# Optimization experiments

Measured on AMD Instinct MI355X. Metric: run time of the kernel, lower is better.

## Reference

```python
import jax, jax.numpy as jnp
import numpy as np


def _outer(a, b):
    # 2D cross product z-component: a.x*b.y - a.y*b.x, elementwise over [..., 2]
    return a[..., 0] * b[..., 1] - a[..., 1] * b[..., 0]


def setup_inputs() -> dict:
    key = jax.random.key(0)
    P, L = 8192, 3072  # paths, points per path; L = 3*C with C curves
    points = jax.random.normal(key, (P, L, 2), dtype=jnp.float32)
    return {"points": points}


def reference(points) -> jnp.ndarray:
    # points: [P, L, 2], L = 3*C. Curve i uses points[3i], [3i+1], [3i+2],
    # and p4 = points[3i+3] (wrapping to points[0] for the last curve).
    p1 = points[:, 0::3]                 # [P, C, 2]
    p2 = points[:, 1::3]                 # [P, C, 2]
    p3 = points[:, 2::3]                 # [P, C, 2]
    p4 = jnp.roll(p1, -1, axis=1)        # [P, C, 2]; wraps last curve to points[0]

    v12 = p2 - p1
    v23 = p3 - p2
    v43 = p4 - p3

    # D1: hard sign test (1 if outer > 0 else 0), matching the torch branch
    D1 = (_outer(v12, v23) > 0).astype(points.dtype)  # [P, C]
    # D2: normalized outer product between first and last control segments
    D2 = _outer(v12, v43) / (
        jnp.linalg.norm(v12, axis=-1) * jnp.linalg.norm(v43, axis=-1)
    )                                                   # [P, C]

    xings = D1 * jax.nn.relu(-D2) + (1.0 - D1) * jax.nn.relu(D2)
    return jnp.mean(xings)
```

## Files before the change

### kernel.cpp

```cpp
#include <hip/hip_runtime.h>


#define NTHREADS 256
#define NBLOCKS  2048
#define ROW_FLOATS 6144
#define ITEMS_PER_ROW 256

__device__ __forceinline__ float xing1(float p1x, float p1y, float p2x, float p2y,
                                       float p3x, float p3y, float p4x, float p4y) {
    float v12x = p2x - p1x, v12y = p2y - p1y;
    float v23x = p3x - p2x, v23y = p3y - p2y;
    float v43x = p4x - p3x, v43y = p4y - p3y;
    float c1 = v12x * v23y - v12y * v23x;
    float c2 = v12x * v43y - v12y * v43x;
    float d12 = v12x * v12x + v12y * v12y;
    float d43 = v43x * v43x + v43y * v43y;
    float inv = __builtin_amdgcn_rsqf(d12 * d43);
    float s = (c1 > 0.0f) ? -c2 : c2;
    return fmaxf(s * inv, 0.0f);
}

__global__ __launch_bounds__(NTHREADS) void xing_partial(const float* __restrict__ pts,
                                                         float* __restrict__ partial,
                                                         int itemsTotal) {
    float acc = 0.0f;
    for (int w = blockIdx.x * NTHREADS + threadIdx.x; w < itemsTotal;
         w += NBLOCKS * NTHREADS) {
        int row = w >> 8;
        int t   = w & (ITEMS_PER_ROW - 1);
        const float* base = pts + (size_t)row * ROW_FLOATS + t * 24;

        float4 q0 = *reinterpret_cast<const float4*>(base);
        float4 q1 = *reinterpret_cast<const float4*>(base + 4);
        float4 q2 = *reinterpret_cast<const float4*>(base + 8);
        float4 q3 = *reinterpret_cast<const float4*>(base + 12);
        float4 q4 = *reinterpret_cast<const float4*>(base + 16);
        float4 q5 = *reinterpret_cast<const float4*>(base + 20);

        int nextOff = (t == ITEMS_PER_ROW - 1) ? 0 : (t * 24 + 24);
        float2 tl = *reinterpret_cast<const float2*>(pts + (size_t)row * ROW_FLOATS + nextOff);

        acc += xing1(q0.x, q0.y, q0.z, q0.w, q1.x, q1.y, q1.z, q1.w);
        acc += xing1(q1.z, q1.w, q2.x, q2.y, q2.z, q2.w, q3.x, q3.y);
        acc += xing1(q3.x, q3.y, q3.z, q3.w, q4.x, q4.y, q4.z, q4.w);
        acc += xing1(q4.z, q4.w, q5.x, q5.y, q5.z, q5.w, tl.x, tl.y);
    }

    for (int off = 32; off > 0; off >>= 1) acc += __shfl_down(acc, off);

    __shared__ float wsum[NTHREADS / 64];
    int lane = threadIdx.x & 63;
    int wid  = threadIdx.x >> 6;
    if (lane == 0) wsum[wid] = acc;
    __syncthreads();
    if (threadIdx.x == 0) {
        float s = 0.0f;
        #pragma unroll
        for (int i = 0; i < NTHREADS / 64; ++i) s += wsum[i];
        partial[blockIdx.x] = s;
    }
}

__global__ __launch_bounds__(NTHREADS) void xing_final(const float* __restrict__ partial,
                                                       float* __restrict__ out,
                                                       int n, float invN) {
    float acc = 0.0f;
    for (int i = threadIdx.x; i < n; i += NTHREADS) acc += partial[i];
    for (int off = 32; off > 0; off >>= 1) acc += __shfl_down(acc, off);

    __shared__ float wsum[NTHREADS / 64];
    int lane = threadIdx.x & 63;
    int wid  = threadIdx.x >> 6;
    if (lane == 0) wsum[wid] = acc;
    __syncthreads();
    if (threadIdx.x == 0) {
        float s = 0.0f;
        #pragma unroll
        for (int i = 0; i < NTHREADS / 64; ++i) s += wsum[i];
        out[0] = s * invN;
    }
}

extern "C" void kernel_launch(void* const* d_in, const int* in_sizes, int n_in,
                              void* d_out, int out_size, void* d_ws, size_t ws_size,
                              hipStream_t stream) {
    const float* pts = (const float*)d_in[0];
    float* out = (float*)d_out;
    float* partial = (float*)d_ws;

    int P = in_sizes[0] / ROW_FLOATS;
    int itemsTotal = P * ITEMS_PER_ROW;
    float invN = 1.0f / (float)((long long)P * 1024);

    xing_partial<<<NBLOCKS, NTHREADS, 0, stream>>>(pts, partial, itemsTotal);
    xing_final<<<1, NTHREADS, 0, stream>>>(partial, out, NBLOCKS, invN);
}
```

Before: 269.4 us.

## Stage each path row through padded LDS for fully coalesced global loads

Each block now loads a whole row with contiguous float4 loads across threads and writes it into padded shared memory, then each thread reads its 24-float strided chunk from LDS. The aim is to replace the per-thread 96-byte strided global reads, which coalesce poorly, with fully coalesced ones. The padding is there to avoid LDS bank conflicts. The cost is two barriers per row and an LDS round trip, which limits load/compute overlap across rows within a block.

```diff
diff --git a/kernel.cpp b/kernel.cpp
--- a/kernel.cpp
+++ b/kernel.cpp
@@ -4,7 +4,9 @@
 #define NTHREADS 256
 #define NBLOCKS  2048
 #define ROW_FLOATS 6144
-#define ITEMS_PER_ROW 256
+#define LDS_WORDS (ROW_FLOATS + (ROW_FLOATS / 32) * 4)
+
+__device__ __forceinline__ int pa(int w) { return w + ((w >> 5) << 2); }
 
 __device__ __forceinline__ float xing1(float p1x, float p1y, float p2x, float p2y,
                                        float p3x, float p3y, float p4x, float p4y) {
@@ -22,38 +24,47 @@
 
 __global__ __launch_bounds__(NTHREADS) void xing_partial(const float* __restrict__ pts,
                                                          float* __restrict__ partial,
-                                                         int itemsTotal) {
+                                                         int P) {
+    __shared__ float lds[LDS_WORDS];
+    const int tid = threadIdx.x;
     float acc = 0.0f;
-    for (int w = blockIdx.x * NTHREADS + threadIdx.x; w < itemsTotal;
-         w += NBLOCKS * NTHREADS) {
-        int row = w >> 8;
-        int t   = w & (ITEMS_PER_ROW - 1);
-        const float* base = pts + (size_t)row * ROW_FLOATS + t * 24;
 
-        float4 q0 = *reinterpret_cast<const float4*>(base);
-        float4 q1 = *reinterpret_cast<const float4*>(base + 4);
-        float4 q2 = *reinterpret_cast<const float4*>(base + 8);
-        float4 q3 = *reinterpret_cast<const float4*>(base + 12);
-        float4 q4 = *reinterpret_cast<const float4*>(base + 16);
-        float4 q5 = *reinterpret_cast<const float4*>(base + 20);
+    for (int row = blockIdx.x; row < P; row += NBLOCKS) {
+        const float4* rowp = reinterpret_cast<const float4*>(pts + (size_t)row * ROW_FLOATS);
 
-        int nextOff = (t == ITEMS_PER_ROW - 1) ? 0 : (t * 24 + 24);
-        float2 tl = *reinterpret_cast<const float2*>(pts + (size_t)row * ROW_FLOATS + nextOff);
+        #pragma unroll
+        for (int i = 0; i < 6; ++i) {
+            int idx = i * NTHREADS + tid;
+            float4 v = rowp[idx];
+            *reinterpret_cast<float4*>(&lds[pa(idx * 4)]) = v;
+        }
+        __syncthreads();
+
+        int a = tid * 24;
+        float4 q0 = *reinterpret_cast<const float4*>(&lds[pa(a)]);
+        float4 q1 = *reinterpret_cast<const float4*>(&lds[pa(a + 4)]);
+        float4 q2 = *reinterpret_cast<const float4*>(&lds[pa(a + 8)]);
+        float4 q3 = *reinterpret_cast<const float4*>(&lds[pa(a + 12)]);
+        float4 q4 = *reinterpret_cast<const float4*>(&lds[pa(a + 16)]);
+        float4 q5 = *reinterpret_cast<const float4*>(&lds[pa(a + 20)]);
+        int an = (tid == NTHREADS - 1) ? 0 : a + 24;
+        float2 tl = *reinterpret_cast<const float2*>(&lds[pa(an)]);
 
         acc += xing1(q0.x, q0.y, q0.z, q0.w, q1.x, q1.y, q1.z, q1.w);
         acc += xing1(q1.z, q1.w, q2.x, q2.y, q2.z, q2.w, q3.x, q3.y);
         acc += xing1(q3.x, q3.y, q3.z, q3.w, q4.x, q4.y, q4.z, q4.w);
         acc += xing1(q4.z, q4.w, q5.x, q5.y, q5.z, q5.w, tl.x, tl.y);
+        __syncthreads();
     }
 
     for (int off = 32; off > 0; off >>= 1) acc += __shfl_down(acc, off);
 
     __shared__ float wsum[NTHREADS / 64];
-    int lane = threadIdx.x & 63;
-    int wid  = threadIdx.x >> 6;
+    int lane = tid & 63;
+    int wid  = tid >> 6;
     if (lane == 0) wsum[wid] = acc;
     __syncthreads();
-    if (threadIdx.x == 0) {
+    if (tid == 0) {
         float s = 0.0f;
         #pragma unroll
         for (int i = 0; i < NTHREADS / 64; ++i) s += wsum[i];
@@ -89,9 +100,8 @@
     float* partial = (float*)d_ws;
 
     int P = in_sizes[0] / ROW_FLOATS;
-    int itemsTotal = P * ITEMS_PER_ROW;
     float invN = 1.0f / (float)((long long)P * 1024);
 
-    xing_partial<<<NBLOCKS, NTHREADS, 0, stream>>>(pts, partial, itemsTotal);
+    xing_partial<<<NBLOCKS, NTHREADS, 0, stream>>>(pts, partial, P);
     xing_final<<<1, NTHREADS, 0, stream>>>(partial, out, NBLOCKS, invN);
 }
```

New measurement: 271.9 us. No clear change (+0.9%).
